# Kernel tuning notes

Hardware: AMD Instinct MI355X
Metric: run time of the kernel (lower is better)

Reference implementation:

```python
import jax, jax.numpy as jnp
import numpy as np

T = 64      # simulation_length
B = 128     # batch
D = 2048    # flattened input dim / axons per core
N = 2048    # neurons per core
L = 4       # number of cores (chain, latency = index)
OUT = 1024  # number of output_sources


def setup_inputs() -> dict:
    key = jax.random.key(0)
    k0, k1, k2, k3 = jax.random.split(key, 4)
    x = jax.random.uniform(k0, (B, D), dtype=jnp.float32)          # rate-coded input in [0,1)
    # core_params[l] = core_matrix.transpose() -> shape [N, A]; scaled for sane membrane dynamics
    W = jax.random.normal(k1, (L, N, D), dtype=jnp.float32) * 0.05
    thresholds = jnp.ones((L,), dtype=jnp.float32)
    # axon_sources: per-core irregular gather indices into previous core's neurons (input for l=0)
    axon_idx = jax.random.randint(k2, (L, D), 0, D, dtype=jnp.int32)
    out_idx = jax.random.randint(k3, (OUT,), 0, N, dtype=jnp.int32)
    return dict(x=x, W=W, thresholds=thresholds, axon_idx=axon_idx,
                out_idx=out_idx, simulation_length=T)


def _ideal_spike_scan(avg, thr, T):
    """Per-cycle: m += avg; spike = (m > thr); m[m > thr] -= thr.  avg: [B, N]."""
    def step(m, _):
        m = m + avg
        s = (m > thr).astype(m.dtype)
        return m - thr * s, s
    _, spikes = jax.lax.scan(step, jnp.zeros_like(avg), None, length=T)
    return spikes  # [T, B, N]


def reference(x, W, thresholds, axon_idx, out_idx, simulation_length):
    T = simulation_length
    L = W.shape[0]
    # generate_input_spike_train: x replicated across all cycles -> cache[-1]
    prev = jnp.broadcast_to(x, (T,) + x.shape)  # [T, B, D]
    for l in range(L):
        # get_signal_tensor: gather axon source signals for every cycle
        gathered = prev[:, :, axon_idx[l]]                    # [T, B, A]
        # per-cycle matmul: torch.matmul(core_params, sig.T).T == sig @ W[l].T
        val = jnp.einsum('tba,na->tbn', gathered, W[l])       # [T, B, N]
        avg = val.mean(axis=0)                                # avg_values [B, N]
        # ideal membrane integrate + threshold-reset recurrence -> out spike train
        prev = _ideal_spike_scan(avg, thresholds[l], T)       # [T, B, N]
    # output_signals: sum of output-source spikes over all cycles
    return prev[:, :, out_idx].sum(axis=0)                    # [B, OUT]
```

## Files before the change

### kernel.cpp

```cpp
#include <hip/hip_runtime.h>

#define BB   128
#define DD   2048
#define NN   2048
#define LL   4
#define OUTN 1024
#define NB   (NN * BB)
#define KC   32
#define PADW 34

typedef double double4v __attribute__((ext_vector_type(4)));

__global__ __launch_bounds__(256) void gather0_kernel(
    const float* __restrict__ x, const int* __restrict__ idx0,
    float* __restrict__ At)
{
    int i = blockIdx.x * 256 + threadIdx.x;
    int k = i >> 7;
    int b = i & 127;
    At[i] = x[b * DD + idx0[k]];
}

__global__ __launch_bounds__(256, 4) void gemm_mfma64(
    const float* __restrict__ srcT,
    const int*   __restrict__ idx,
    const float* __restrict__ Wl,
    double*      __restrict__ parts,
    int krange)
{
    __shared__ __align__(16) double Wq[64 * PADW];

    const int t     = threadIdx.x;
    const int nsup  = blockIdx.x;
    const int bsup  = blockIdx.y;
    const int split = blockIdx.z;
    const int n0b   = nsup * 64;
    const int k0s   = split * krange;
    const int wq    = t >> 6;
    const int lane  = t & 63;
    const int q     = lane >> 4;
    const int c     = lane & 15;
    const int b0w   = bsup * 64 + wq * 16;

    double4v pr = {0., 0., 0., 0.}, pc = {0., 0., 0., 0.};
    pr = __builtin_amdgcn_mfma_f64_16x16x4f64(0.25 * (double)c, 1.0, pr, 0, 0, 0);
    pc = __builtin_amdgcn_mfma_f64_16x16x4f64(0.25, (double)c, pc, 0, 0, 0);
    int rowD[4], colD[4];
    #pragma unroll
    for (int r = 0; r < 4; ++r) {
        rowD[r] = (int)(pr[r] + 0.25);
        colD[r] = (int)(pc[r] + 0.25);
    }

    const int sn = t >> 3;
    const int sm = t & 7;

    double4v acc[4] = {{0.,0.,0.,0.},{0.,0.,0.,0.},{0.,0.,0.,0.},{0.,0.,0.,0.}};

    float4 a0 = *(const float4*)(Wl + (size_t)(n0b + sn) * DD + k0s + 4 * sm);
    float4 a1 = *(const float4*)(Wl + (size_t)(n0b + sn + 32) * DD + k0s + 4 * sm);
    float bF[8];
    #pragma unroll
    for (int j = 0; j < 8; ++j) {
        int k = k0s + 4 * j + q;
        int row = idx ? idx[k] : k;
        bF[j] = srcT[(size_t)row * BB + b0w + c];
    }

    const int nchunk = krange / KC;
    for (int ch = 0; ch < nchunk; ++ch) {
        __syncthreads();
        {
            const float* f0 = (const float*)&a0;
            const float* f1 = (const float*)&a1;
            double* w0 = Wq + sn * PADW + sm;
            double* w1 = Wq + (sn + 32) * PADW + sm;
            #pragma unroll
            for (int i = 0; i < 4; ++i) {
                w0[i * 8] = (double)f0[i];
                w1[i * 8] = (double)f1[i];
            }
        }
        if (ch + 1 < nchunk) {
            const float* p = Wl + (size_t)(n0b + sn) * DD + k0s + (ch + 1) * KC + 4 * sm;
            a0 = *(const float4*)p;
            a1 = *(const float4*)(p + (size_t)32 * DD);
        }
        __syncthreads();

        float bN[8];
        if (ch + 1 < nchunk) {
            int k0n = k0s + (ch + 1) * KC;
            #pragma unroll
            for (int j = 0; j < 8; ++j) {
                int k = k0n + 4 * j + q;
                int row = idx ? idx[k] : k;
                bN[j] = srcT[(size_t)row * BB + b0w + c];
            }
        }

        #pragma unroll
        for (int jp = 0; jp < 4; ++jp) {
            double2 wf[4];
            #pragma unroll
            for (int tt = 0; tt < 4; ++tt)
                wf[tt] = *(const double2*)(Wq + (16 * tt + c) * PADW + q * 8 + 2 * jp);
            double bv0 = (double)bF[2 * jp];
            double bv1 = (double)bF[2 * jp + 1];
            #pragma unroll
            for (int tt = 0; tt < 4; ++tt)
                acc[tt] = __builtin_amdgcn_mfma_f64_16x16x4f64(wf[tt].x, bv0, acc[tt], 0, 0, 0);
            #pragma unroll
            for (int tt = 0; tt < 4; ++tt)
                acc[tt] = __builtin_amdgcn_mfma_f64_16x16x4f64(wf[tt].y, bv1, acc[tt], 0, 0, 0);
        }
        if (ch + 1 < nchunk) {
            #pragma unroll
            for (int j = 0; j < 8; ++j) bF[j] = bN[j];
        }
    }

    #pragma unroll
    for (int tt = 0; tt < 4; ++tt) {
        #pragma unroll
        for (int r = 0; r < 4; ++r) {
            int n = n0b + 16 * tt + rowD[r];
            size_t o = ((size_t)split * NN + n) * BB + b0w + colD[r];
            parts[o] = acc[tt][r];
        }
    }
}

__global__ __launch_bounds__(256) void spike_kernel(
    const double* __restrict__ parts, const float* __restrict__ thresholds,
    int l, const int* __restrict__ Tptr,
    float* __restrict__ meanT, float* __restrict__ cntT, int nsplit)
{
    int i0 = blockIdx.x * 256 + threadIdx.x;
    int i1 = i0 + NB / 2;
    double a0 = 0.0, a1 = 0.0;
    for (int s = 0; s < nsplit; ++s) {
        a0 += parts[(size_t)s * NB + i0];
        a1 += parts[(size_t)s * NB + i1];
    }
    const double thr = (double)thresholds[l];
    const int T = *Tptr;
    double m0 = 0.0, m1 = 0.0;
    int c0 = 0, c1 = 0;
    for (int t = 0; t < T; ++t) {
        m0 += a0;
        m1 += a1;
        if (m0 > thr) { c0++; m0 -= thr; }
        if (m1 > thr) { c1++; m1 -= thr; }
    }
    if (l == LL - 1) {
        cntT[i0] = (float)c0;
        cntT[i1] = (float)c1;
    } else {
        meanT[i0] = (float)c0 / (float)T;
        meanT[i1] = (float)c1 / (float)T;
    }
}

__global__ __launch_bounds__(256) void out_kernel(
    const float* __restrict__ cntT, const int* __restrict__ out_idx,
    float* __restrict__ out)
{
    int i = blockIdx.x * 256 + threadIdx.x;
    int b = i >> 10;
    int o = i & 1023;
    out[i] = cntT[(size_t)out_idx[o] * BB + b];
}

extern "C" void kernel_launch(void* const* d_in, const int* in_sizes, int n_in,
                              void* d_out, int out_size, void* d_ws, size_t ws_size,
                              hipStream_t stream)
{
    const float* x    = (const float*)d_in[0];
    const float* W    = (const float*)d_in[1];
    const float* thr  = (const float*)d_in[2];
    const int*   axon = (const int*)d_in[3];
    const int*   oidx = (const int*)d_in[4];
    const int*   Tptr = (const int*)d_in[5];
    float* out = (float*)d_out;

    char* ws = (char*)d_ws;
    float*  At    = (float*)ws;
    float*  meanT = (float*)(ws + (1u << 20));
    float*  cntT  = (float*)(ws + (2u << 20));
    double* parts = (double*)(ws + (3u << 20));

    int nsplit = 16;
    while (nsplit > 1 &&
           (size_t)nsplit * NB * sizeof(double) + (3u << 20) > ws_size)
        nsplit >>= 1;
    const int krange = DD / nsplit;

    gather0_kernel<<<(DD * BB) / 256, 256, 0, stream>>>(x, axon, At);

    for (int l = 0; l < LL; ++l) {
        const float* srcT = (l == 0) ? At : meanT;
        const int*   idx  = (l == 0) ? nullptr : (axon + (size_t)l * DD);
        gemm_mfma64<<<dim3(NN / 64, BB / 64, nsplit), 256, 0, stream>>>(
            srcT, idx, W + (size_t)l * NN * DD, parts, krange);
        spike_kernel<<<NB / 512, 256, 0, stream>>>(
            parts, thr, l, Tptr, meanT, cntT, nsplit);
    }

    out_kernel<<<(BB * OUTN) / 256, 256, 0, stream>>>(cntT, oidx, out);
}
```

Before: 243.0 us.

## Double-buffer shared W tile and prefetch two chunks ahead in GEMM

Converts the GEMM's shared-memory W tile into a double buffer so the next chunk's fp64 tile is written while the current chunk's MFMAs run, removing one of the two barriers per chunk. Global loads of W and gathered activations are prefetched two chunks ahead. This doubles LDS use per block (about 34 KB) and adds register pressure, which may reduce occupancy under launch bounds of 4 blocks per CU.

```diff
diff --git a/kernel.cpp b/kernel.cpp
--- a/kernel.cpp
+++ b/kernel.cpp
@@ -28,7 +28,7 @@
     double*      __restrict__ parts,
     int krange)
 {
-    __shared__ __align__(16) double Wq[64 * PADW];
+    __shared__ __align__(16) double Wq[2][64 * PADW];
 
     const int t     = threadIdx.x;
     const int nsup  = blockIdx.x;
@@ -57,40 +57,80 @@
 
     double4v acc[4] = {{0.,0.,0.,0.},{0.,0.,0.,0.},{0.,0.,0.,0.},{0.,0.,0.,0.}};
 
+    const int nchunk = krange / KC;
+
     float4 a0 = *(const float4*)(Wl + (size_t)(n0b + sn) * DD + k0s + 4 * sm);
     float4 a1 = *(const float4*)(Wl + (size_t)(n0b + sn + 32) * DD + k0s + 4 * sm);
-    float bF[8];
+    float bF[8], bN[8];
     #pragma unroll
     for (int j = 0; j < 8; ++j) {
         int k = k0s + 4 * j + q;
         int row = idx ? idx[k] : k;
         bF[j] = srcT[(size_t)row * BB + b0w + c];
     }
-
-    const int nchunk = krange / KC;
+    {
+        const float* f0 = (const float*)&a0;
+        const float* f1 = (const float*)&a1;
+        double* w0 = Wq[0] + sn * PADW + sm;
+        double* w1 = Wq[0] + (sn + 32) * PADW + sm;
+        #pragma unroll
+        for (int i = 0; i < 4; ++i) {
+            w0[i * 8] = (double)f0[i];
+            w1[i * 8] = (double)f1[i];
+        }
+    }
+    if (nchunk > 1) {
+        const float* p = Wl + (size_t)(n0b + sn) * DD + k0s + KC + 4 * sm;
+        a0 = *(const float4*)p;
+        a1 = *(const float4*)(p + (size_t)32 * DD);
+        #pragma unroll
+        for (int j = 0; j < 8; ++j) {
+            int k = k0s + KC + 4 * j + q;
+            int row = idx ? idx[k] : k;
+            bN[j] = srcT[(size_t)row * BB + b0w + c];
+        }
+    }
+    __syncthreads();
+
     for (int ch = 0; ch < nchunk; ++ch) {
-        __syncthreads();
-        {
+        double* buf = Wq[ch & 1];
+        if (ch + 1 < nchunk) {
             const float* f0 = (const float*)&a0;
             const float* f1 = (const float*)&a1;
-            double* w0 = Wq + sn * PADW + sm;
-            double* w1 = Wq + (sn + 32) * PADW + sm;
+            double* w0 = Wq[(ch + 1) & 1] + sn * PADW + sm;
+            double* w1 = Wq[(ch + 1) & 1] + (sn + 32) * PADW + sm;
             #pragma unroll
             for (int i = 0; i < 4; ++i) {
                 w0[i * 8] = (double)f0[i];
                 w1[i * 8] = (double)f1[i];
             }
         }
-        if (ch + 1 < nchunk) {
-            const float* p = Wl + (size_t)(n0b + sn) * DD + k0s + (ch + 1) * KC + 4 * sm;
+        if (ch + 2 < nchunk) {
+            const float* p = Wl + (size_t)(n0b + sn) * DD + k0s + (ch + 2) * KC + 4 * sm;
             a0 = *(const float4*)p;
             a1 = *(const float4*)(p + (size_t)32 * DD);
         }
-        __syncthreads();
-
-        float bN[8];
-        if (ch + 1 < nchunk) {
-            int k0n = k0s + (ch + 1) * KC;
+
+        #pragma unroll
+        for (int jp = 0; jp < 4; ++jp) {
+            double2 wf[4];
+            #pragma unroll
+            for (int tt = 0; tt < 4; ++tt)
+                wf[tt] = *(const double2*)(buf + (16 * tt + c) * PADW + q * 8 + 2 * jp);
+            double bv0 = (double)bF[2 * jp];
+            double bv1 = (double)bF[2 * jp + 1];
+            #pragma unroll
+            for (int tt = 0; tt < 4; ++tt)
+                acc[tt] = __builtin_amdgcn_mfma_f64_16x16x4f64(wf[tt].x, bv0, acc[tt], 0, 0, 0);
+            #pragma unroll
+            for (int tt = 0; tt < 4; ++tt)
+                acc[tt] = __builtin_amdgcn_mfma_f64_16x16x4f64(wf[tt].y, bv1, acc[tt], 0, 0, 0);
+        }
+
+        #pragma unroll
+        for (int j = 0; j < 8; ++j) bF[j] = bN[j];
+        if (ch + 2 < nchunk) {
+            int k0n = k0s + (ch + 2) * KC;
             #pragma unroll
             for (int j = 0; j < 8; ++j) {
                 int k = k0n + 4 * j + q;
@@ -98,26 +138,7 @@
                 bN[j] = srcT[(size_t)row * BB + b0w + c];
             }
         }
-
-        #pragma unroll
-        for (int jp = 0; jp < 4; ++jp) {
-            double2 wf[4];
-            #pragma unroll
-            for (int tt = 0; tt < 4; ++tt)
-                wf[tt] = *(const double2*)(Wq + (16 * tt + c) * PADW + q * 8 + 2 * jp);
-            double bv0 = (double)bF[2 * jp];
-            double bv1 = (double)bF[2 * jp + 1];
-            #pragma unroll
-            for (int tt = 0; tt < 4; ++tt)
-                acc[tt] = __builtin_amdgcn_mfma_f64_16x16x4f64(wf[tt].x, bv0, acc[tt], 0, 0, 0);
-            #pragma unroll
-            for (int tt = 0; tt < 4; ++tt)
-                acc[tt] = __builtin_amdgcn_mfma_f64_16x16x4f64(wf[tt].y, bv1, acc[tt], 0, 0, 0);
-        }
-        if (ch + 1 < nchunk) {
-            #pragma unroll
-            for (int j = 0; j < 8; ++j) bF[j] = bN[j];
-        }
+        __syncthreads();
     }
 
     #pragma unroll
```

After: 249.0 us. +2.5%, slower.
